# Kernel tuning notes

Measured on AMD Instinct MI355X. Metric: run time of the kernel, lower is better.

The kernel has to match this reference:

```python
import jax, jax.numpy as jnp
import numpy as np

NUM_DOCS = 1_000_000
VOCAB = 30522
NNZ_PER_ROW = 64
NNZ = NUM_DOCS * NNZ_PER_ROW
Q_NNZ = 32
SHARDS = 4
TOP_K = 100


def setup_inputs() -> dict:
    key = jax.random.key(0)
    k1, k2, k3, k4 = jax.random.split(key, 4)
    doc_values = jax.random.uniform(k1, (NNZ,), dtype=jnp.float32)          # CSR values (impact weights)
    doc_indices = jax.random.randint(k2, (NNZ,), 0, VOCAB, dtype=jnp.int32)  # CSR column indices
    row_ids = (jnp.arange(NNZ, dtype=jnp.int32) // NNZ_PER_ROW)              # expanded crow -> sorted row ids
    q_indices = jax.random.randint(k3, (Q_NNZ,), 0, VOCAB, dtype=jnp.int32)
    q_values = jax.random.uniform(k4, (Q_NNZ,), dtype=jnp.float32)
    return {
        "doc_values": doc_values,
        "q_values": q_values,
        "doc_indices": doc_indices,
        "row_ids": row_ids,
        "q_indices": q_indices,
    }


def reference(doc_values, q_values, doc_indices, row_ids, q_indices):
    # build_dense_query: sparse COO -> dense (duplicates coalesced by summation)
    query = jnp.zeros((VOCAB,), dtype=doc_values.dtype).at[q_indices].add(q_values)
    # CSR SpMV: per-nnz contribution gathered from query, summed per row
    contrib = doc_values * query[doc_indices]                                 # [NNZ]
    scores = jax.ops.segment_sum(contrib, row_ids, num_segments=NUM_DOCS,
                                 indices_are_sorted=True)                     # [NUM_DOCS]
    # per-shard top-k (equal row split, matching _split_csr)
    rows_per_shard = NUM_DOCS // SHARDS
    shard_scores = scores.reshape(SHARDS, rows_per_shard)
    loc_s, loc_i = jax.lax.top_k(shard_scores, TOP_K)                         # [SHARDS, K]
    offsets = (jnp.arange(SHARDS, dtype=loc_i.dtype) * rows_per_shard)[:, None]
    all_scores = loc_s.reshape(-1)                                            # [SHARDS*K]
    all_indices = (loc_i + offsets).reshape(-1)
    # merge_topk_results: global top-k over concatenated shard candidates
    top_scores, sel = jax.lax.top_k(all_scores, TOP_K)
    top_indices = all_indices[sel]
    return top_scores, top_indices
```

## Files before the change

### kernel.cpp

```cpp
#include <hip/hip_runtime.h>

#define NUM_DOCS 1000000
#define VOCAB 30522
#define NNZ 64000000LL
#define Q_NNZ 32
#define TOP_K 100
#define CAND_MAX 4096
#define BM_WORDS 954

#define OFF_Q       0
#define OFF_HIST    30528
#define OFF_PART    (OFF_HIST + 65536)
#define OFF_DONE    (OFF_PART + 256)
#define OFF_COUNTER (OFF_DONE + 1)
#define OFF_THRESH  (OFF_COUNTER + 1)
#define OFF_CTRLEND (OFF_THRESH + 13)
#define OFF_CANDS   OFF_CTRLEND
#define OFF_CANDI   (OFF_CANDS + CAND_MAX)
#define OFF_SCORES  (OFF_CANDI + CAND_MAX)
#define ZERO_WORDS  OFF_CTRLEND

__global__ void scatter_q_kernel(const float* __restrict__ qv, const int* __restrict__ qi,
                                 float* __restrict__ q) {
    int i = threadIdx.x;
    if (i < Q_NNZ) atomicAdd(&q[qi[i]], qv[i]);
}

__global__ __launch_bounds__(256) void score_kernel(
        const float* __restrict__ dv, const int* __restrict__ di,
        const int* __restrict__ qi, const float* __restrict__ qg,
        float* __restrict__ scores, unsigned* __restrict__ hist) {
    __shared__ unsigned bm[BM_WORDS];
    for (int i = threadIdx.x; i < BM_WORDS; i += 256) bm[i] = 0u;
    __syncthreads();
    if (threadIdx.x < Q_NNZ) {
        int v = qi[threadIdx.x];
        atomicOr(&bm[v >> 5], 1u << (v & 31));
    }
    __syncthreads();

    int t = blockIdx.x * 256 + threadIdx.x;
    long long base = (long long)t * 4;
    int4 x = *(const int4*)(di + base);
    float s = 0.f;
    if ((bm[x.x >> 5] >> (x.x & 31)) & 1u) s += dv[base + 0] * qg[x.x];
    if ((bm[x.y >> 5] >> (x.y & 31)) & 1u) s += dv[base + 1] * qg[x.y];
    if ((bm[x.z >> 5] >> (x.z & 31)) & 1u) s += dv[base + 2] * qg[x.z];
    if ((bm[x.w >> 5] >> (x.w & 31)) & 1u) s += dv[base + 3] * qg[x.w];
    s += __shfl_xor(s, 1);
    s += __shfl_xor(s, 2);
    s += __shfl_xor(s, 4);
    s += __shfl_xor(s, 8);
    if ((threadIdx.x & 15) == 0) {
        int doc = t >> 4;
        scores[doc] = s;
        if (s > 0.f) atomicAdd(&hist[__float_as_uint(s) >> 16], 1u);
    }
}

__global__ __launch_bounds__(256) void thresh_kernel(
        const unsigned* __restrict__ hist, unsigned* __restrict__ part,
        unsigned* __restrict__ done, unsigned* __restrict__ thresh) {
    int b = blockIdx.x, t = threadIdx.x;
    unsigned v = hist[b * 256 + t];
    unsigned s = v;
    for (int off = 1; off < 64; off <<= 1) s += __shfl_xor(s, off);
    __shared__ unsigned wsum[4];
    if ((t & 63) == 0) wsum[t >> 6] = s;
    __syncthreads();
    if (t == 0) {
        atomicAdd(&part[b], wsum[0] + wsum[1] + wsum[2] + wsum[3]);
        __threadfence();
    }
    __shared__ int lastflag;
    if (t == 0) lastflag = (atomicAdd(done, 1u) == 255u) ? 1 : 0;
    __syncthreads();
    if (!lastflag) return;

    __shared__ unsigned parts[256];
    parts[t] = atomicAdd(&part[t], 0u);
    __syncthreads();
    __shared__ int sc;
    __shared__ unsigned scum;
    if (t == 0) {
        unsigned cum = 0;
        int c = 255;
        for (; c >= 0; --c) {
            if (cum + parts[c] >= TOP_K) break;
            cum += parts[c];
        }
        sc = c; scum = cum;
    }
    __syncthreads();
    int c = sc;
    __shared__ unsigned bins[256];
    if (c >= 0) bins[t] = hist[c * 256 + t];
    __syncthreads();
    if (t == 0) {
        unsigned bin = 1;
        if (c >= 0) {
            unsigned cum = scum;
            int b2 = 255;
            for (; b2 >= 0; --b2) {
                cum += bins[b2];
                if (cum >= TOP_K) break;
            }
            if (b2 < 0) b2 = 0;
            bin = (unsigned)(c * 256 + b2);
        }
        thresh[0] = bin << 16;
    }
}

__global__ void gather_kernel(const float* __restrict__ scores, const unsigned* __restrict__ thresh,
                              unsigned* __restrict__ counter,
                              float* __restrict__ cs, int* __restrict__ ci) {
    int i = blockIdx.x * blockDim.x + threadIdx.x;
    if (i < NUM_DOCS) {
        float s = scores[i];
        if (__float_as_uint(s) >= thresh[0]) {
            unsigned p = atomicAdd(counter, 1u);
            if (p < CAND_MAX) { cs[p] = s; ci[p] = i; }
        }
    }
}

__global__ void topk_kernel(const unsigned* __restrict__ counter,
                            const float* __restrict__ cs, const int* __restrict__ ci,
                            float* __restrict__ out) {
    __shared__ float ls[CAND_MAX];
    __shared__ int   li[CAND_MAX];
    int n = (int)min(counter[0], (unsigned)CAND_MAX);
    for (int i = threadIdx.x; i < n; i += 64) { ls[i] = cs[i]; li[i] = ci[i]; }
    __syncthreads();
    for (int k = 0; k < TOP_K; ++k) {
        float best = -1.f; int bestd = 0x7fffffff; int bestp = -1;
        for (int i = threadIdx.x; i < n; i += 64) {
            float s = ls[i];
            int   d = li[i];
            if (s > best || (s == best && d < bestd)) { best = s; bestd = d; bestp = i; }
        }
        for (int off = 1; off < 64; off <<= 1) {
            float os = __shfl_xor(best,  off);
            int   od = __shfl_xor(bestd, off);
            int   op = __shfl_xor(bestp, off);
            if (os > best || (os == best && od < bestd)) { best = os; bestd = od; bestp = op; }
        }
        if (threadIdx.x == 0) {
            out[k]         = (bestp >= 0) ? best : 0.f;
            out[TOP_K + k] = (float)((bestp >= 0) ? bestd : 0);
            if (bestp >= 0) ls[bestp] = -1.f;
        }
        __syncthreads();
    }
}

extern "C" void kernel_launch(void* const* d_in, const int* in_sizes, int n_in,
                              void* d_out, int out_size, void* d_ws, size_t ws_size,
                              hipStream_t stream) {
    const float* doc_values  = (const float*)d_in[0];
    const float* q_values    = (const float*)d_in[1];
    const int*   doc_indices = (const int*)d_in[2];
    const int*   q_indices   = (const int*)d_in[4];
    float* out = (float*)d_out;

    float*    ws      = (float*)d_ws;
    float*    q       = ws + OFF_Q;
    unsigned* hist    = (unsigned*)d_ws + OFF_HIST;
    unsigned* part    = (unsigned*)d_ws + OFF_PART;
    unsigned* done    = (unsigned*)d_ws + OFF_DONE;
    unsigned* counter = (unsigned*)d_ws + OFF_COUNTER;
    unsigned* thresh  = (unsigned*)d_ws + OFF_THRESH;
    float*    cs      = ws + OFF_CANDS;
    int*      ci      = (int*)d_ws + OFF_CANDI;
    float*    scores  = ws + OFF_SCORES;

    hipMemsetAsync(d_ws, 0, (size_t)ZERO_WORDS * 4, stream);

    scatter_q_kernel<<<1, 64, 0, stream>>>(q_values, q_indices, q);

    score_kernel<<<62500, 256, 0, stream>>>(doc_values, doc_indices, q_indices, q, scores, hist);

    thresh_kernel<<<256, 256, 0, stream>>>(hist, part, done, thresh);

    int blocks1m = (NUM_DOCS + 255) / 256;
    gather_kernel<<<blocks1m, 256, 0, stream>>>(scores, thresh, counter, cs, ci);
    topk_kernel<<<1, 64, 0, stream>>>(counter, cs, ci, out);
}
```

Before: 649.0 us.

## Fuse candidate emission into scoring and drop scatter and gather passes

The separate query-scatter kernel is removed; each scoring block keeps the query in shared memory and coalesces duplicate indices with a linear scan on bitmap hits. Scoring now appends every positive-scoring doc to one of 64 per-slot candidate buffers instead of writing a full 1M score array, so the gather pass over all scores disappears. A single 1024-thread select kernel filters the candidates by threshold and runs the top-k. Index loads use nontemporal hints. The risk is that a slot holding more than 4096 positive docs (about 15.6k docs per slot here) silently drops candidates, and the per-hit atomics on shared slot counters can contend.

```diff
diff --git a/kernel.cpp b/kernel.cpp
--- a/kernel.cpp
+++ b/kernel.cpp
@@ -5,56 +5,66 @@
 #define NNZ 64000000LL
 #define Q_NNZ 32
 #define TOP_K 100
-#define CAND_MAX 4096
 #define BM_WORDS 954
+#define NSLOT 64
+#define CAND_SEG 4096
+#define FCAP 2048
 
-#define OFF_Q       0
-#define OFF_HIST    30528
-#define OFF_PART    (OFF_HIST + 65536)
+typedef int   v4i __attribute__((ext_vector_type(4)));
+
+#define OFF_HIST    0
+#define OFF_PART    65536
 #define OFF_DONE    (OFF_PART + 256)
-#define OFF_COUNTER (OFF_DONE + 1)
-#define OFF_THRESH  (OFF_COUNTER + 1)
-#define OFF_CTRLEND (OFF_THRESH + 13)
-#define OFF_CANDS   OFF_CTRLEND
-#define OFF_CANDI   (OFF_CANDS + CAND_MAX)
-#define OFF_SCORES  (OFF_CANDI + CAND_MAX)
-#define ZERO_WORDS  OFF_CTRLEND
-
-__global__ void scatter_q_kernel(const float* __restrict__ qv, const int* __restrict__ qi,
-                                 float* __restrict__ q) {
-    int i = threadIdx.x;
-    if (i < Q_NNZ) atomicAdd(&q[qi[i]], qv[i]);
-}
+#define OFF_THRESH  (OFF_DONE + 1)
+#define OFF_CNT     (OFF_THRESH + 15)
+#define OFF_CANDS   (OFF_CNT + NSLOT)
+#define OFF_CANDI   (OFF_CANDS + NSLOT*CAND_SEG)
+#define ZERO_WORDS  OFF_CANDS
 
 __global__ __launch_bounds__(256) void score_kernel(
         const float* __restrict__ dv, const int* __restrict__ di,
-        const int* __restrict__ qi, const float* __restrict__ qg,
-        float* __restrict__ scores, unsigned* __restrict__ hist) {
+        const int* __restrict__ qi, const float* __restrict__ qv,
+        unsigned* __restrict__ hist, unsigned* __restrict__ cnt,
+        float* __restrict__ cs, int* __restrict__ ci) {
     __shared__ unsigned bm[BM_WORDS];
+    __shared__ int   qiS[Q_NNZ];
+    __shared__ float qvS[Q_NNZ];
     for (int i = threadIdx.x; i < BM_WORDS; i += 256) bm[i] = 0u;
     __syncthreads();
     if (threadIdx.x < Q_NNZ) {
         int v = qi[threadIdx.x];
+        qiS[threadIdx.x] = v;
+        qvS[threadIdx.x] = qv[threadIdx.x];
         atomicOr(&bm[v >> 5], 1u << (v & 31));
     }
     __syncthreads();
 
     int t = blockIdx.x * 256 + threadIdx.x;
     long long base = (long long)t * 4;
-    int4 x = *(const int4*)(di + base);
+    v4i x = __builtin_nontemporal_load((const v4i*)(di + base));
     float s = 0.f;
-    if ((bm[x.x >> 5] >> (x.x & 31)) & 1u) s += dv[base + 0] * qg[x.x];
-    if ((bm[x.y >> 5] >> (x.y & 31)) & 1u) s += dv[base + 1] * qg[x.y];
-    if ((bm[x.z >> 5] >> (x.z & 31)) & 1u) s += dv[base + 2] * qg[x.z];
-    if ((bm[x.w >> 5] >> (x.w & 31)) & 1u) s += dv[base + 3] * qg[x.w];
+#define ELEM(xx, off)                                                   \
+    if ((bm[(xx) >> 5] >> ((xx) & 31)) & 1u) {                          \
+        float qs = 0.f;                                                 \
+        for (int j = 0; j < Q_NNZ; ++j)                                 \
+            if (qiS[j] == (xx)) qs += qvS[j];                           \
+        s += dv[base + (off)] * qs;                                     \
+    }
+    ELEM(x.x, 0) ELEM(x.y, 1) ELEM(x.z, 2) ELEM(x.w, 3)
+#undef ELEM
     s += __shfl_xor(s, 1);
     s += __shfl_xor(s, 2);
     s += __shfl_xor(s, 4);
     s += __shfl_xor(s, 8);
-    if ((threadIdx.x & 15) == 0) {
+    if ((threadIdx.x & 15) == 0 && s > 0.f) {
         int doc = t >> 4;
-        scores[doc] = s;
-        if (s > 0.f) atomicAdd(&hist[__float_as_uint(s) >> 16], 1u);
+        atomicAdd(&hist[__float_as_uint(s) >> 16], 1u);
+        int slot = blockIdx.x & (NSLOT - 1);
+        unsigned p = atomicAdd(&cnt[slot], 1u);
+        if (p < CAND_SEG) {
+            cs[slot * CAND_SEG + p] = s;
+            ci[slot * CAND_SEG + p] = doc;
+        }
     }
 }
 
@@ -62,8 +72,7 @@
         const unsigned* __restrict__ hist, unsigned* __restrict__ part,
         unsigned* __restrict__ done, unsigned* __restrict__ thresh) {
     int b = blockIdx.x, t = threadIdx.x;
-    unsigned v = hist[b * 256 + t];
-    unsigned s = v;
+    unsigned s = hist[b * 256 + t];
     for (int off = 1; off < 64; off <<= 1) s += __shfl_xor(s, off);
     __shared__ unsigned wsum[4];
     if ((t & 63) == 0) wsum[t >> 6] = s;
@@ -112,32 +121,37 @@
     }
 }
 
-__global__ void gather_kernel(const float* __restrict__ scores, const unsigned* __restrict__ thresh,
-                              unsigned* __restrict__ counter,
-                              float* __restrict__ cs, int* __restrict__ ci) {
-    int i = blockIdx.x * blockDim.x + threadIdx.x;
-    if (i < NUM_DOCS) {
-        float s = scores[i];
-        if (__float_as_uint(s) >= thresh[0]) {
-            unsigned p = atomicAdd(counter, 1u);
-            if (p < CAND_MAX) { cs[p] = s; ci[p] = i; }
+__global__ __launch_bounds__(1024) void select_kernel(
+        const unsigned* __restrict__ cnt, const unsigned* __restrict__ thresh,
+        const float* __restrict__ cs, const int* __restrict__ ci,
+        float* __restrict__ out) {
+    __shared__ float fs[FCAP];
+    __shared__ int   fi[FCAP];
+    __shared__ int   m;
+    __shared__ int   ns[NSLOT];
+    int t = threadIdx.x;
+    if (t == 0) m = 0;
+    if (t < NSLOT) ns[t] = (int)min(cnt[t], (unsigned)CAND_SEG);
+    __syncthreads();
+    unsigned th = thresh[0];
+    for (int slot = 0; slot < NSLOT; ++slot) {
+        int n = ns[slot];
+        for (int i = t; i < n; i += 1024) {
+            float s = cs[slot * CAND_SEG + i];
+            if (__float_as_uint(s) >= th) {
+                int p = atomicAdd(&m, 1);
+                if (p < FCAP) { fs[p] = s; fi[p] = ci[slot * CAND_SEG + i]; }
+            }
         }
     }
-}
-
-__global__ void topk_kernel(const unsigned* __restrict__ counter,
-                            const float* __restrict__ cs, const int* __restrict__ ci,
-                            float* __restrict__ out) {
-    __shared__ float ls[CAND_MAX];
-    __shared__ int   li[CAND_MAX];
-    int n = (int)min(counter[0], (unsigned)CAND_MAX);
-    for (int i = threadIdx.x; i < n; i += 64) { ls[i] = cs[i]; li[i] = ci[i]; }
     __syncthreads();
+    if (t >= 64) return;
+    int n = min(m, FCAP);
     for (int k = 0; k < TOP_K; ++k) {
         float best = -1.f; int bestd = 0x7fffffff; int bestp = -1;
-        for (int i = threadIdx.x; i < n; i += 64) {
-            float s = ls[i];
-            int   d = li[i];
+        for (int i = t; i < n; i += 64) {
+            float s = fs[i];
+            int   d = fi[i];
             if (s > best || (s == best && d < bestd)) { best = s; bestd = d; bestp = i; }
         }
         for (int off = 1; off < 64; off <<= 1) {
@@ -146,10 +160,10 @@
             int   op = __shfl_xor(bestp, off);
             if (os > best || (os == best && od < bestd)) { best = os; bestd = od; bestp = op; }
         }
-        if (threadIdx.x == 0) {
+        if (t == 0) {
             out[k]         = (bestp >= 0) ? best : 0.f;
             out[TOP_K + k] = (float)((bestp >= 0) ? bestd : 0);
-            if (bestp >= 0) ls[bestp] = -1.f;
+            if (bestp >= 0) fs[bestp] = -1.f;
         }
         __syncthreads();
     }
@@ -164,26 +178,18 @@
     const int*   q_indices   = (const int*)d_in[4];
     float* out = (float*)d_out;
 
-    float*    ws      = (float*)d_ws;
-    float*    q       = ws + OFF_Q;
-    unsigned* hist    = (unsigned*)d_ws + OFF_HIST;
-    unsigned* part    = (unsigned*)d_ws + OFF_PART;
-    unsigned* done    = (unsigned*)d_ws + OFF_DONE;
-    unsigned* counter = (unsigned*)d_ws + OFF_COUNTER;
-    unsigned* thresh  = (unsigned*)d_ws + OFF_THRESH;
-    float*    cs      = ws + OFF_CANDS;
-    int*      ci      = (int*)d_ws + OFF_CANDI;
-    float*    scores  = ws + OFF_SCORES;
+    unsigned* hist   = (unsigned*)d_ws + OFF_HIST;
+    unsigned* part   = (unsigned*)d_ws + OFF_PART;
+    unsigned* done   = (unsigned*)d_ws + OFF_DONE;
+    unsigned* thresh = (unsigned*)d_ws + OFF_THRESH;
+    unsigned* cnt    = (unsigned*)d_ws + OFF_CNT;
+    float*    cs     = (float*)d_ws + OFF_CANDS;
+    int*      ci     = (int*)d_ws + OFF_CANDI;
 
     hipMemsetAsync(d_ws, 0, (size_t)ZERO_WORDS * 4, stream);
 
-    scatter_q_kernel<<<1, 64, 0, stream>>>(q_values, q_indices, q);
-
-    score_kernel<<<62500, 256, 0, stream>>>(doc_values, doc_indices, q_indices, q, scores, hist);
-
+    score_kernel<<<62500, 256, 0, stream>>>(doc_values, doc_indices, q_indices, q_values,
+                                            hist, cnt, cs, ci);
     thresh_kernel<<<256, 256, 0, stream>>>(hist, part, done, thresh);
-
-    int blocks1m = (NUM_DOCS + 255) / 256;
-    gather_kernel<<<blocks1m, 256, 0, stream>>>(scores, thresh, counter, cs, ci);
-    topk_kernel<<<1, 64, 0, stream>>>(counter, cs, ci, out);
+    select_kernel<<<1, 1024, 0, stream>>>(cnt, thresh, cs, ci, out);
 }
```

After: 838.6 us. 1.29x slower.
